# Kernel tuning notes

Hardware: AMD Instinct MI355X
Metric: run time of the kernel (lower is better)

## Reference

```python
import jax, jax.numpy as jnp
import numpy as np

D = 768      # hidden_size
H = 12       # num_head
HD = D // H  # head_dim
LN_EPS = 1e-5


def setup_inputs() -> dict:
    key = jax.random.key(0)
    ks = jax.random.split(key, 9)
    N, S = 4, 2048
    s = 0.02
    return {
        "hidden_state": jax.random.normal(ks[0], (N, S, D), dtype=jnp.float32),
        "key_padding_mask": jax.random.randint(ks[1], (N, S), 0, 2, dtype=jnp.int64),
        "Wq": jax.random.normal(ks[2], (D, D), dtype=jnp.float32) * s,
        "Wk": jax.random.normal(ks[3], (D, D), dtype=jnp.float32) * s,
        "Wv": jax.random.normal(ks[4], (D, D), dtype=jnp.float32) * s,
        "Wo": jax.random.normal(ks[5], (D, D), dtype=jnp.float32) * s,
        "W1": jax.random.normal(ks[6], (4 * D, D), dtype=jnp.float32) * s,
        "W2": jax.random.normal(ks[7], (D, 4 * D), dtype=jnp.float32) * s,
        "ln_g": jnp.ones((D,), dtype=jnp.float32),
        "ln_b": jnp.zeros((D,), dtype=jnp.float32),
    }


def _layernorm(x, g, b):
    mu = jnp.mean(x, axis=-1, keepdims=True)
    var = jnp.mean(jnp.square(x - mu), axis=-1, keepdims=True)
    return (x - mu) * jax.lax.rsqrt(var + LN_EPS) * g + b


def reference(hidden_state, key_padding_mask, Wq, Wk, Wv, Wo, W1, W2, ln_g, ln_b):
    x = hidden_state
    N, S, _ = x.shape
    # Note: original module projects K and V from `query` (self-attention).
    def proj(W):
        return (x @ W.T).reshape(N, S, H, HD).transpose(0, 2, 1, 3)  # [N,H,S,HD]
    Q, K, V = proj(Wq), proj(Wk), proj(Wv)
    scores = jnp.einsum("bhqd,bhkd->bhqk", Q, K)  # [N,H,S,S]
    # int mask: 0 marks padding positions -> masked with -inf
    pad = (key_padding_mask == 0)[:, None, None, :]  # [N,1,1,S]
    scores = jnp.where(pad, -jnp.inf, scores)
    attn = jax.nn.softmax(scores / np.sqrt(HD), axis=-1)
    ctx = jnp.einsum("bhqk,bhkd->bhqd", attn, V)
    ctx = ctx.transpose(0, 2, 1, 3).reshape(N, S, D)
    mha = ctx @ Wo.T
    # residual + LayerNorm (same LN params used twice, as in the original)
    n1 = _layernorm(x + mha, ln_g, ln_b)
    # FFN with exact GELU (torch nn.GELU default)
    f = jax.nn.gelu(n1 @ W1.T, approximate=False) @ W2.T
    return _layernorm(n1 + f, ln_g, ln_b)
```

## Files before the change

kernel.cpp:

```cpp
#include <hip/hip_runtime.h>
#include <math.h>

typedef unsigned short u16;
typedef unsigned int u32;
typedef __bf16 bf16x8 __attribute__((ext_vector_type(8)));
typedef float f32x4 __attribute__((ext_vector_type(4)));
typedef u32 u32x4 __attribute__((ext_vector_type(4)));

#define NB 4
#define SS 2048
#define DD 768
#define HH 12
#define HD 64
#define ROWS (NB*SS)

__device__ __forceinline__ u16 f2bf(float f) {
    union { float f; unsigned u; } v; v.f = f;
    unsigned r = v.u + 0x7fffu + ((v.u >> 16) & 1u);
    return (u16)(r >> 16);
}
__device__ __forceinline__ u32 fas(float f) { union { float f; u32 u; } v; v.f = f; return v.u; }

__device__ __forceinline__ void gl_lds16(const void* g, void* l) {
    __builtin_amdgcn_global_load_lds((__attribute__((address_space(1))) void*)(g),
                                     (__attribute__((address_space(3))) void*)(l),
                                     16, 0, 0);
}

__global__ __launch_bounds__(256) void prep_kernel(
        const float* __restrict__ X, const float* __restrict__ Wq,
        const float* __restrict__ Wk, const float* __restrict__ Wv,
        const float* __restrict__ Wo, const float* __restrict__ W1,
        const float* __restrict__ W2,
        u16* __restrict__ Xb, u16* __restrict__ Wqkvb, u16* __restrict__ Wob,
        u16* __restrict__ W1b, u16* __restrict__ W2b) {
    const int blk = blockIdx.x, tid = threadIdx.x;
    const float* src; u16* dst; int idx;
    if (blk < 6144)       { src = X;  dst = Xb;               idx = blk * 1024 + tid * 4; }
    else if (blk < 6720)  { src = Wq; dst = Wqkvb;            idx = (blk - 6144) * 1024 + tid * 4; }
    else if (blk < 7296)  { src = Wk; dst = Wqkvb + DD * DD;  idx = (blk - 6720) * 1024 + tid * 4; }
    else if (blk < 7872)  { src = Wv; dst = Wqkvb + 2*DD*DD;  idx = (blk - 7296) * 1024 + tid * 4; }
    else if (blk < 8448)  { src = Wo; dst = Wob;              idx = (blk - 7872) * 1024 + tid * 4; }
    else if (blk < 10752) { src = W1; dst = W1b;              idx = (blk - 8448) * 1024 + tid * 4; }
    else                  { src = W2; dst = W2b;              idx = (blk - 10752) * 1024 + tid * 4; }
    float4 v = *(const float4*)&src[idx];
    ushort4 o;
    o.x = f2bf(v.x); o.y = f2bf(v.y); o.z = f2bf(v.z); o.w = f2bf(v.w);
    *(ushort4*)&dst[idx] = o;
}

__global__ __launch_bounds__(256) void scan_kernel(const int* __restrict__ mask,
                                                   int* __restrict__ cidx,
                                                   int* __restrict__ cnt) {
    const int b = blockIdx.x, tid = threadIdx.x;
    const int lane = tid & 63, wave = tid >> 6;
    const int base = b * SS + tid * 8;
    int4 m0 = *(const int4*)&mask[base];
    int4 m1 = *(const int4*)&mask[base + 4];
    int v[8] = { m0.x != 0, m0.y != 0, m0.z != 0, m0.w != 0,
                 m1.x != 0, m1.y != 0, m1.z != 0, m1.w != 0 };
    int own = 0;
#pragma unroll
    for (int i = 0; i < 8; ++i) own += v[i];
    int inc = own;
#pragma unroll
    for (int o = 1; o < 64; o <<= 1) {
        int n = __shfl_up(inc, o);
        if (lane >= o) inc += n;
    }
    __shared__ int wsum[4];
    if (lane == 63) wsum[wave] = inc;
    __syncthreads();
    int wbase = 0;
#pragma unroll
    for (int w = 0; w < 4; ++w) wbase += (w < wave) ? wsum[w] : 0;
    int pos = wbase + inc - own;
    int o8[8];
#pragma unroll
    for (int i = 0; i < 8; ++i) { o8[i] = v[i] ? pos : -1; pos += v[i]; }
    *(int4*)&cidx[base]     = make_int4(o8[0], o8[1], o8[2], o8[3]);
    *(int4*)&cidx[base + 4] = make_int4(o8[4], o8[5], o8[6], o8[7]);
    if (tid == 255) cnt[b] = wbase + inc;
}

template <int EPI, int BN>
__global__ __launch_bounds__(256) void gemm_bt(const u16* __restrict__ A,
                                               const u16* __restrict__ B,
                                               int M, int N, int K,
                                               void* __restrict__ out,
                                               const void* __restrict__ aux,
                                               u16* __restrict__ Qb,
                                               u16* __restrict__ Kb,
                                               u16* __restrict__ Vb,
                                               const int* __restrict__ cidx) {
    __shared__ __align__(16) u16 lA[128 * 64];
    __shared__ __align__(16) u16 lB[BN * 64];
    constexpr int MI = (BN == 128) ? 4 : 2;
    const int tid = threadIdx.x;
    const int lane = tid & 63, wave = tid >> 6;
    const int quad = lane >> 4, lc = lane & 15;
    const int xcd = blockIdx.x & 7, loc = blockIdx.x >> 3;
    const int mb = xcd * 8 + (loc & 7), nb = loc >> 3;
    const int m0 = mb * 128, n0 = nb * BN;
    const int wrow = (BN == 128) ? (wave >> 1) * 64 : wave * 32;
    const int wcol = (BN == 128) ? (wave & 1) * 64 : 0;
    const int swz = lc & 7;

    f32x4 acc[MI][4] = {};

    for (int kb = 0; kb < K; kb += 64) {
        __syncthreads();
#pragma unroll
        for (int p0 = 0; p0 < 1024; p0 += 256) {
            int p = p0 + tid, row = p >> 3, cl = (p & 7) ^ (row & 7);
            gl_lds16(A + (size_t)(m0 + row) * K + kb + cl * 8, &lA[(size_t)(p0 + wave * 64) * 8]);
        }
#pragma unroll
        for (int p0 = 0; p0 < BN * 8; p0 += 256) {
            int p = p0 + tid, row = p >> 3, cl = (p & 7) ^ (row & 7);
            gl_lds16(B + (size_t)(n0 + row) * K + kb + cl * 8, &lB[(size_t)(p0 + wave * 64) * 8]);
        }
        __syncthreads();
#pragma unroll
        for (int k2 = 0; k2 < 2; ++k2) {
            bf16x8 af[MI], bfr[4];
#pragma unroll
            for (int t = 0; t < MI; ++t)
                af[t] = *(const bf16x8*)&lA[(wrow + t * 16 + lc) * 64 + ((quad + k2 * 4) ^ swz) * 8];
#pragma unroll
            for (int t = 0; t < 4; ++t)
                bfr[t] = *(const bf16x8*)&lB[(wcol + t * 16 + lc) * 64 + ((quad + k2 * 4) ^ swz) * 8];
#pragma unroll
            for (int mi = 0; mi < MI; ++mi)
#pragma unroll
                for (int ni = 0; ni < 4; ++ni)
                    acc[mi][ni] = __builtin_amdgcn_mfma_f32_16x16x32_bf16(af[mi], bfr[ni],
                                                                         acc[mi][ni], 0, 0, 0);
        }
    }

#pragma unroll
    for (int mi = 0; mi < MI; ++mi) {
        int csa[4];
        if constexpr (EPI == 0) {
            int mbase = m0 + wrow + mi * 16 + quad * 4;
            int4 cs4 = *(const int4*)&cidx[(mbase >> 11) * SS + (mbase & 2047)];
            csa[0] = cs4.x; csa[1] = cs4.y; csa[2] = cs4.z; csa[3] = cs4.w;
        }
#pragma unroll
        for (int r = 0; r < 4; ++r) {
            int m = m0 + wrow + mi * 16 + quad * 4 + r;
#pragma unroll
            for (int ni = 0; ni < 4; ++ni) {
                int n = n0 + wcol + ni * 16 + lc;
                float v = acc[mi][ni][r];
                if constexpr (EPI == 0) {
                    int b = m >> 11, s = m & 2047;
                    int which = n / DD, rem = n - which * DD;
                    int h = rem >> 6, d = rem & 63;
                    u16* dst = which == 0 ? Qb : (which == 1 ? Kb : Vb);
                    int sidx = which == 0 ? s : csa[r];
                    if (sidx >= 0)
                        dst[((((size_t)b * HH + h) * SS + sidx) << 6) + d] = f2bf(v);
                } else if constexpr (EPI == 1) {
                    float u = v * fmaf(v * v, 0.035677408f, 0.7978845608f);
                    float e = __builtin_amdgcn_exp2f(u * 2.885390082f);
                    float g = v - v * __builtin_amdgcn_rcpf(e + 1.0f);
                    ((u16*)out)[(size_t)m * N + n] = f2bf(g);
                } else if constexpr (EPI == 2) {
                    ((float*)out)[(size_t)m * N + n] =
                        v + ((const float*)aux)[(size_t)m * N + n];
                } else {
                    ((float*)out)[(size_t)m * N + n] =
                        v + (float)(((const __bf16*)aux)[(size_t)m * N + n]);
                }
            }
        }
    }
}

__global__ __launch_bounds__(256) void transpose_v(const u16* __restrict__ V,
                                                   u16* __restrict__ Vt,
                                                   const int* __restrict__ cnt) {
    __shared__ u16 t[32][33];
    int bh = blockIdx.z;
    int c = cnt[bh / HH];
    int cr = (c + 63) & ~63;
    int s0 = blockIdx.x * 32, d0 = blockIdx.y * 32;
    if (s0 >= cr) return;
    const u16* vb = V + (size_t)bh * SS * HD;
    u16* vtb = Vt + (size_t)bh * HD * SS;
    int tx = threadIdx.x & 31, ty = threadIdx.x >> 5;
#pragma unroll
    for (int i = 0; i < 32; i += 8) {
        int s = s0 + ty + i;
        t[ty + i][tx] = (s < c) ? vb[(size_t)s * HD + d0 + tx] : (u16)0;
    }
    __syncthreads();
#pragma unroll
    for (int i = 0; i < 32; i += 8) vtb[(size_t)(d0 + ty + i) * SS + s0 + tx] = t[tx][ty + i];
}

__global__ __launch_bounds__(256, 3) void attn_kernel(const u16* __restrict__ Q,
                                                      const u16* __restrict__ K,
                                                      const u16* __restrict__ Vt,
                                                      const int* __restrict__ cntg,
                                                      u16* __restrict__ Ctx) {
    __shared__ __align__(16) u16 lK[2][4096];
    __shared__ __align__(16) u16 lV[2][4096];
    const int tid = threadIdx.x, lane = tid & 63, wave = tid >> 6;
    const int quad = lane >> 4, lc = lane & 15;
    const int bh = blockIdx.x % (NB * HH);
    const int b = bh / HH, h = bh - b * HH;
    const int q0 = (blockIdx.x / (NB * HH)) * 128;
    const u16* Qg = Q + ((size_t)bh * SS + q0 + wave * 32) * HD;
    const u16* Kg = K + (size_t)bh * SS * HD;
    const u16* Vg = Vt + (size_t)bh * HD * SS;
    const int sw = lc & 7;
    const int cnt = cntg[b];
    const int nt = (cnt + 63) >> 6;

    const int srow = tid >> 3, scl = (tid & 7) ^ (srow & 7);
    const int srow2 = (256 + tid) >> 3, scl2 = (tid & 7) ^ (srow2 & 7);

    auto stage = [&](int bi, int j0) {
        gl_lds16(Kg + (size_t)(j0 + srow) * HD + scl * 8,   &lK[bi][(size_t)(wave * 64) * 8]);
        gl_lds16(Kg + (size_t)(j0 + srow2) * HD + scl2 * 8, &lK[bi][(size_t)(256 + wave * 64) * 8]);
        gl_lds16(Vg + (size_t)srow * SS + j0 + scl * 8,     &lV[bi][(size_t)(wave * 64) * 8]);
        gl_lds16(Vg + (size_t)srow2 * SS + j0 + scl2 * 8,   &lV[bi][(size_t)(256 + wave * 64) * 8]);
    };

    bf16x8 qf[2][2];
#pragma unroll
    for (int mi = 0; mi < 2; ++mi)
#pragma unroll
        for (int k2 = 0; k2 < 2; ++k2)
            qf[mi][k2] = *(const bf16x8*)(Qg + (size_t)(mi * 16 + lc) * HD + k2 * 32 + quad * 8);

    bf16x8 onesf;
#pragma unroll
    for (int i = 0; i < 8; ++i) onesf[i] = (__bf16)1.0f;

    f32x4 oacc[2][4] = {};
    f32x4 lsum[2] = {};

    stage(0, 0);
    for (int t = 0; t < nt; ++t) {
        const int cur = t & 1;
        if (t < nt - 1) {
            stage(cur ^ 1, (t + 1) * 64);
            __builtin_amdgcn_sched_barrier(0);
            asm volatile("s_waitcnt vmcnt(4)" ::: "memory");
        } else {
            __builtin_amdgcn_sched_barrier(0);
            asm volatile("s_waitcnt vmcnt(0)" ::: "memory");
        }
        __builtin_amdgcn_sched_barrier(0);
        __builtin_amdgcn_s_barrier();
        __builtin_amdgcn_sched_barrier(0);

        const u16* bK = &lK[cur][0];
        const u16* bV = &lV[cur][0];

        f32x4 sacc[2][4] = {};
        __builtin_amdgcn_s_setprio(1);
#pragma unroll
        for (int k2 = 0; k2 < 2; ++k2) {
            bf16x8 kf[4];
#pragma unroll
            for (int ni = 0; ni < 4; ++ni)
                kf[ni] = *(const bf16x8*)&bK[(ni * 16 + lc) * 64 + ((quad + k2 * 4) ^ sw) * 8];
#pragma unroll
            for (int ni = 0; ni < 4; ++ni) {
                sacc[0][ni] = __builtin_amdgcn_mfma_f32_16x16x32_bf16(kf[ni], qf[0][k2], sacc[0][ni], 0, 0, 0);
                sacc[1][ni] = __builtin_amdgcn_mfma_f32_16x16x32_bf16(kf[ni], qf[1][k2], sacc[1][ni], 0, 0, 0);
            }
        }
        __builtin_amdgcn_s_setprio(0);

        const int kb_ = cnt - t * 64;
        const bool part = kb_ < 64;
        u32 pa[2][4], pb[2][4];
#pragma unroll
        for (int ni = 0; ni < 4; ++ni) {
#pragma unroll
            for (int mi = 0; mi < 2; ++mi) {
#pragma unroll
                for (int r = 0; r < 4; ++r) {
                    float e = __builtin_amdgcn_exp2f(sacc[mi][ni][r] * 0.180336880f);
                    if (part) e = (ni * 16 + quad * 4 + r < kb_) ? e : 0.0f;
                    sacc[mi][ni][r] = e;
                }
                pa[mi][ni] = __builtin_amdgcn_perm(fas(sacc[mi][ni][1]), fas(sacc[mi][ni][0]), 0x07060302);
                pb[mi][ni] = __builtin_amdgcn_perm(fas(sacc[mi][ni][3]), fas(sacc[mi][ni][2]), 0x07060302);
            }
        }

        bf16x8 pf[2][2];
#pragma unroll
        for (int mi = 0; mi < 2; ++mi)
#pragma unroll
            for (int k2 = 0; k2 < 2; ++k2) {
                u32 xa = pa[mi][2 * k2], ya = pa[mi][2 * k2 + 1];
                u32 xb = pb[mi][2 * k2], yb = pb[mi][2 * k2 + 1];
                asm("v_permlane32_swap_b32 %0, %1" : "+v"(xa), "+v"(ya));
                asm("v_permlane16_swap_b32 %0, %1" : "+v"(xa), "+v"(ya));
                asm("v_permlane32_swap_b32 %0, %1" : "+v"(xb), "+v"(yb));
                asm("v_permlane16_swap_b32 %0, %1" : "+v"(xb), "+v"(yb));
                u32x4 pw = { xa, xb, ya, yb };
                pf[mi][k2] = __builtin_bit_cast(bf16x8, pw);
            }

        __builtin_amdgcn_s_setprio(1);
#pragma unroll
        for (int k2 = 0; k2 < 2; ++k2) {
            lsum[0] = __builtin_amdgcn_mfma_f32_16x16x32_bf16(pf[0][k2], onesf, lsum[0], 0, 0, 0);
            lsum[1] = __builtin_amdgcn_mfma_f32_16x16x32_bf16(pf[1][k2], onesf, lsum[1], 0, 0, 0);
#pragma unroll
            for (int ni = 0; ni < 4; ++ni) {
                bf16x8 vf = *(const bf16x8*)&bV[(ni * 16 + lc) * 64 + ((quad + k2 * 4) ^ sw) * 8];
                oacc[0][ni] = __builtin_amdgcn_mfma_f32_16x16x32_bf16(pf[0][k2], vf, oacc[0][ni], 0, 0, 0);
                oacc[1][ni] = __builtin_amdgcn_mfma_f32_16x16x32_bf16(pf[1][k2], vf, oacc[1][ni], 0, 0, 0);
            }
        }
        __builtin_amdgcn_s_setprio(0);

        __builtin_amdgcn_sched_barrier(0);
        __builtin_amdgcn_s_barrier();
    }

#pragma unroll
    for (int mi = 0; mi < 2; ++mi)
#pragma unroll
        for (int r = 0; r < 4; ++r) {
            float inv = 1.0f / lsum[mi][r];
            int s = q0 + wave * 32 + mi * 16 + quad * 4 + r;
            size_t base = ((size_t)(b * SS + s)) * DD + h * HD;
#pragma unroll
            for (int ni = 0; ni < 4; ++ni)
                Ctx[base + ni * 16 + lc] = f2bf(oacc[mi][ni][r] * inv);
        }
}

__global__ __launch_bounds__(256) void ln_kernel(const float* __restrict__ in,
                                                 const float* __restrict__ g,
                                                 const float* __restrict__ bb,
                                                 u16* __restrict__ out_bf,
                                                 float* __restrict__ out_f) {
    const int row = blockIdx.x, tid = threadIdx.x;
    const float* x = in + (size_t)row * DD;
    float v0 = x[tid], v1 = x[tid + 256], v2 = x[tid + 512];
    float s = v0 + v1 + v2;
    float q = v0 * v0 + v1 * v1 + v2 * v2;
#pragma unroll
    for (int o = 1; o < 64; o <<= 1) {
        s += __shfl_xor(s, o);
        q += __shfl_xor(q, o);
    }
    __shared__ float rs[4], rq[4];
    int wave = tid >> 6;
    if ((tid & 63) == 0) { rs[wave] = s; rq[wave] = q; }
    __syncthreads();
    s = rs[0] + rs[1] + rs[2] + rs[3];
    q = rq[0] + rq[1] + rq[2] + rq[3];
    float mu = s * (1.0f / DD);
    float var = q * (1.0f / DD) - mu * mu;
    float rstd = rsqrtf(var + 1e-5f);
#pragma unroll
    for (int j = 0; j < 3; ++j) {
        int col = tid + j * 256;
        float v = (j == 0 ? v0 : (j == 1 ? v1 : v2));
        float y = (v - mu) * rstd * g[col] + bb[col];
        if (out_bf) out_bf[(size_t)row * DD + col] = f2bf(y);
        if (out_f) out_f[(size_t)row * DD + col] = y;
    }
}

extern "C" void kernel_launch(void* const* d_in, const int* in_sizes, int n_in,
                              void* d_out, int out_size, void* d_ws, size_t ws_size,
                              hipStream_t stream) {
    const float* X    = (const float*)d_in[0];
    const int*   mask = (const int*)d_in[1];
    const float* Wq   = (const float*)d_in[2];
    const float* Wk   = (const float*)d_in[3];
    const float* Wv   = (const float*)d_in[4];
    const float* Wo   = (const float*)d_in[5];
    const float* W1   = (const float*)d_in[6];
    const float* W2   = (const float*)d_in[7];
    const float* ln_g = (const float*)d_in[8];
    const float* ln_b = (const float*)d_in[9];
    float* out = (float*)d_out;

    char* ws = (char*)d_ws;
    size_t off = 0;
    auto alloc = [&](size_t bytes) {
        void* p = ws + off;
        off += (bytes + 255) & ~(size_t)255;
        return p;
    };
    u16*   Xbf   = (u16*)alloc((size_t)ROWS * DD * 2);
    u16*   Wqkvb = (u16*)alloc((size_t)3 * DD * DD * 2);
    u16*   Wob   = (u16*)alloc((size_t)DD * DD * 2);
    u16*   W1b   = (u16*)alloc((size_t)4 * DD * DD * 2);
    u16*   W2b   = (u16*)alloc((size_t)4 * DD * DD * 2);
    int*   cidx  = (int*)alloc((size_t)NB * SS * 4);
    int*   cnt   = (int*)alloc(256);
    u16*   Qb    = (u16*)alloc((size_t)ROWS * DD * 2);
    u16*   Kb    = (u16*)alloc((size_t)ROWS * DD * 2);
    u16*   Vb    = (u16*)alloc((size_t)ROWS * DD * 2);
    u16*   Vtb   = (u16*)alloc((size_t)ROWS * DD * 2);
    float* resid = (float*)alloc((size_t)ROWS * DD * 4);
    u16*   n1b   = (u16*)alloc((size_t)ROWS * DD * 2);
    u16*   Gb    = Qb;
    u16*   Ctxb  = Xbf;
    float* h2    = resid;

    prep_kernel<<<dim3(13056), dim3(256), 0, stream>>>(
        X, Wq, Wk, Wv, Wo, W1, W2,
        Xbf, Wqkvb, Wob, W1b, W2b);

    scan_kernel<<<dim3(NB), dim3(256), 0, stream>>>(mask, cidx, cnt);

    gemm_bt<0, 128><<<dim3((3 * DD / 128) * (ROWS / 128)), dim3(256), 0, stream>>>(
        Xbf, Wqkvb, ROWS, 3 * DD, DD, nullptr, nullptr, Qb, Kb, Vb, cidx);

    transpose_v<<<dim3(SS / 32, HD / 32, NB * HH), dim3(256), 0, stream>>>(Vb, Vtb, cnt);

    attn_kernel<<<dim3((SS / 128) * (NB * HH)), dim3(256), 0, stream>>>(
        Qb, Kb, Vtb, cnt, Ctxb);

    gemm_bt<2, 64><<<dim3((DD / 64) * (ROWS / 128)), dim3(256), 0, stream>>>(
        Ctxb, Wob, ROWS, DD, DD, resid, X, nullptr, nullptr, nullptr, nullptr);

    ln_kernel<<<dim3(ROWS), dim3(256), 0, stream>>>(resid, ln_g, ln_b, n1b, nullptr);

    gemm_bt<1, 128><<<dim3((4 * DD / 128) * (ROWS / 128)), dim3(256), 0, stream>>>(
        n1b, W1b, ROWS, 4 * DD, DD, Gb, nullptr, nullptr, nullptr, nullptr, nullptr);

    gemm_bt<3, 64><<<dim3((DD / 64) * (ROWS / 128)), dim3(256), 0, stream>>>(
        Gb, W2b, ROWS, DD, 4 * DD, h2, n1b, nullptr, nullptr, nullptr, nullptr);

    ln_kernel<<<dim3(ROWS), dim3(256), 0, stream>>>(h2, ln_g, ln_b, nullptr, out);
}
```

Baseline: 337.3 us.

## Double-buffer GEMM LDS tiles with async prefetch and fold mask scan into prep

The GEMM main loop now uses two LDS buffers. The next K-tile is issued via global_load_lds before computing the current one, with explicit vmcnt waits, barriers, and raised wave priority around the MFMA block. This is meant to hide global-to-LDS latency that the single-buffer loop exposed. The mask prefix-scan also moves into extra blocks of the prep kernel, removing one launch. The cost is double the LDS per block, which may lower occupancy, and hand-counted vmcnt values that must match the number of loads issued per stage.

```diff
diff --git a/kernel.cpp b/kernel.cpp
--- a/kernel.cpp
+++ b/kernel.cpp
@@ -31,9 +31,10 @@
         const float* __restrict__ X, const float* __restrict__ Wq,
         const float* __restrict__ Wk, const float* __restrict__ Wv,
         const float* __restrict__ Wo, const float* __restrict__ W1,
-        const float* __restrict__ W2,
+        const float* __restrict__ W2, const int* __restrict__ mask,
         u16* __restrict__ Xb, u16* __restrict__ Wqkvb, u16* __restrict__ Wob,
-        u16* __restrict__ W1b, u16* __restrict__ W2b) {
+        u16* __restrict__ W1b, u16* __restrict__ W2b,
+        int* __restrict__ cidx, int* __restrict__ cnt) {
     const int blk = blockIdx.x, tid = threadIdx.x;
     const float* src; u16* dst; int idx;
     if (blk < 6144)       { src = X;  dst = Xb;               idx = blk * 1024 + tid * 4; }
@@ -42,45 +43,43 @@
     else if (blk < 7872)  { src = Wv; dst = Wqkvb + 2*DD*DD;  idx = (blk - 7296) * 1024 + tid * 4; }
     else if (blk < 8448)  { src = Wo; dst = Wob;              idx = (blk - 7872) * 1024 + tid * 4; }
     else if (blk < 10752) { src = W1; dst = W1b;              idx = (blk - 8448) * 1024 + tid * 4; }
-    else                  { src = W2; dst = W2b;              idx = (blk - 10752) * 1024 + tid * 4; }
+    else if (blk < 13056) { src = W2; dst = W2b;              idx = (blk - 10752) * 1024 + tid * 4; }
+    else {
+        const int b = blk - 13056;
+        const int lane = tid & 63, wave = tid >> 6;
+        const int base = b * SS + tid * 8;
+        int4 m0 = *(const int4*)&mask[base];
+        int4 m1 = *(const int4*)&mask[base + 4];
+        int v[8] = { m0.x != 0, m0.y != 0, m0.z != 0, m0.w != 0,
+                     m1.x != 0, m1.y != 0, m1.z != 0, m1.w != 0 };
+        int own = 0;
+#pragma unroll
+        for (int i = 0; i < 8; ++i) own += v[i];
+        int inc = own;
+#pragma unroll
+        for (int o = 1; o < 64; o <<= 1) {
+            int n = __shfl_up(inc, o);
+            if (lane >= o) inc += n;
+        }
+        __shared__ int wsum[4];
+        if (lane == 63) wsum[wave] = inc;
+        __syncthreads();
+        int wbase = 0;
+#pragma unroll
+        for (int w = 0; w < 4; ++w) wbase += (w < wave) ? wsum[w] : 0;
+        int pos = wbase + inc - own;
+        int o8[8];
+#pragma unroll
+        for (int i = 0; i < 8; ++i) { o8[i] = v[i] ? pos : -1; pos += v[i]; }
+        *(int4*)&cidx[base]     = make_int4(o8[0], o8[1], o8[2], o8[3]);
+        *(int4*)&cidx[base + 4] = make_int4(o8[4], o8[5], o8[6], o8[7]);
+        if (tid == 255) cnt[b] = wbase + inc;
+        return;
+    }
     float4 v = *(const float4*)&src[idx];
     ushort4 o;
     o.x = f2bf(v.x); o.y = f2bf(v.y); o.z = f2bf(v.z); o.w = f2bf(v.w);
     *(ushort4*)&dst[idx] = o;
-}
-
-__global__ __launch_bounds__(256) void scan_kernel(const int* __restrict__ mask,
-                                                   int* __restrict__ cidx,
-                                                   int* __restrict__ cnt) {
-    const int b = blockIdx.x, tid = threadIdx.x;
-    const int lane = tid & 63, wave = tid >> 6;
-    const int base = b * SS + tid * 8;
-    int4 m0 = *(const int4*)&mask[base];
-    int4 m1 = *(const int4*)&mask[base + 4];
-    int v[8] = { m0.x != 0, m0.y != 0, m0.z != 0, m0.w != 0,
-                 m1.x != 0, m1.y != 0, m1.z != 0, m1.w != 0 };
-    int own = 0;
-#pragma unroll
-    for (int i = 0; i < 8; ++i) own += v[i];
-    int inc = own;
-#pragma unroll
-    for (int o = 1; o < 64; o <<= 1) {
-        int n = __shfl_up(inc, o);
-        if (lane >= o) inc += n;
-    }
-    __shared__ int wsum[4];
-    if (lane == 63) wsum[wave] = inc;
-    __syncthreads();
-    int wbase = 0;
-#pragma unroll
-    for (int w = 0; w < 4; ++w) wbase += (w < wave) ? wsum[w] : 0;
-    int pos = wbase + inc - own;
-    int o8[8];
-#pragma unroll
-    for (int i = 0; i < 8; ++i) { o8[i] = v[i] ? pos : -1; pos += v[i]; }
-    *(int4*)&cidx[base]     = make_int4(o8[0], o8[1], o8[2], o8[3]);
-    *(int4*)&cidx[base + 4] = make_int4(o8[4], o8[5], o8[6], o8[7]);
-    if (tid == 255) cnt[b] = wbase + inc;
 }
 
 template <int EPI, int BN>
@@ -93,8 +92,8 @@
                                                u16* __restrict__ Kb,
                                                u16* __restrict__ Vb,
                                                const int* __restrict__ cidx) {
-    __shared__ __align__(16) u16 lA[128 * 64];
-    __shared__ __align__(16) u16 lB[BN * 64];
+    __shared__ __align__(16) u16 lA[2][128 * 64];
+    __shared__ __align__(16) u16 lB[2][BN * 64];
     constexpr int MI = (BN == 128) ? 4 : 2;
     const int tid = threadIdx.x;
     const int lane = tid & 63, wave = tid >> 6;
@@ -106,37 +105,60 @@
     const int wcol = (BN == 128) ? (wave & 1) * 64 : 0;
     const int swz = lc & 7;
 
-    f32x4 acc[MI][4] = {};
-
-    for (int kb = 0; kb < K; kb += 64) {
-        __syncthreads();
+    auto stage = [&](int bi, int kb) {
 #pragma unroll
         for (int p0 = 0; p0 < 1024; p0 += 256) {
             int p = p0 + tid, row = p >> 3, cl = (p & 7) ^ (row & 7);
-            gl_lds16(A + (size_t)(m0 + row) * K + kb + cl * 8, &lA[(size_t)(p0 + wave * 64) * 8]);
+            gl_lds16(A + (size_t)(m0 + row) * K + kb + cl * 8, &lA[bi][(size_t)(p0 + wave * 64) * 8]);
         }
 #pragma unroll
         for (int p0 = 0; p0 < BN * 8; p0 += 256) {
             int p = p0 + tid, row = p >> 3, cl = (p & 7) ^ (row & 7);
-            gl_lds16(B + (size_t)(n0 + row) * K + kb + cl * 8, &lB[(size_t)(p0 + wave * 64) * 8]);
-        }
-        __syncthreads();
+            gl_lds16(B + (size_t)(n0 + row) * K + kb + cl * 8, &lB[bi][(size_t)(p0 + wave * 64) * 8]);
+        }
+    };
+
+    f32x4 acc[MI][4] = {};
+    const int KT = K >> 6;
+
+    stage(0, 0);
+    for (int t = 0; t < KT; ++t) {
+        const int cur = t & 1;
+        if (t < KT - 1) {
+            stage(cur ^ 1, (t + 1) << 6);
+            __builtin_amdgcn_sched_barrier(0);
+            if constexpr (BN == 128) asm volatile("s_waitcnt vmcnt(8)" ::: "memory");
+            else                     asm volatile("s_waitcnt vmcnt(6)" ::: "memory");
+        } else {
+            __builtin_amdgcn_sched_barrier(0);
+            asm volatile("s_waitcnt vmcnt(0)" ::: "memory");
+        }
+        __builtin_amdgcn_sched_barrier(0);
+        __builtin_amdgcn_s_barrier();
+        __builtin_amdgcn_sched_barrier(0);
+
+        const u16* bA = &lA[cur][0];
+        const u16* bB = &lB[cur][0];
 #pragma unroll
         for (int k2 = 0; k2 < 2; ++k2) {
             bf16x8 af[MI], bfr[4];
 #pragma unroll
-            for (int t = 0; t < MI; ++t)
-                af[t] = *(const bf16x8*)&lA[(wrow + t * 16 + lc) * 64 + ((quad + k2 * 4) ^ swz) * 8];
-#pragma unroll
-            for (int t = 0; t < 4; ++t)
-                bfr[t] = *(const bf16x8*)&lB[(wcol + t * 16 + lc) * 64 + ((quad + k2 * 4) ^ swz) * 8];
+            for (int t_ = 0; t_ < MI; ++t_)
+                af[t_] = *(const bf16x8*)&bA[(wrow + t_ * 16 + lc) * 64 + ((quad + k2 * 4) ^ swz) * 8];
+#pragma unroll
+            for (int t_ = 0; t_ < 4; ++t_)
+                bfr[t_] = *(const bf16x8*)&bB[(wcol + t_ * 16 + lc) * 64 + ((quad + k2 * 4) ^ swz) * 8];
+            __builtin_amdgcn_s_setprio(1);
 #pragma unroll
             for (int mi = 0; mi < MI; ++mi)
 #pragma unroll
                 for (int ni = 0; ni < 4; ++ni)
                     acc[mi][ni] = __builtin_amdgcn_mfma_f32_16x16x32_bf16(af[mi], bfr[ni],
                                                                          acc[mi][ni], 0, 0, 0);
-        }
+            __builtin_amdgcn_s_setprio(0);
+        }
+        __builtin_amdgcn_sched_barrier(0);
+        __builtin_amdgcn_s_barrier();
     }
 
 #pragma unroll
@@ -415,11 +437,9 @@
     u16*   Ctxb  = Xbf;
     float* h2    = resid;
 
-    prep_kernel<<<dim3(13056), dim3(256), 0, stream>>>(
-        X, Wq, Wk, Wv, Wo, W1, W2,
-        Xbf, Wqkvb, Wob, W1b, W2b);
-
-    scan_kernel<<<dim3(NB), dim3(256), 0, stream>>>(mask, cidx, cnt);
+    prep_kernel<<<dim3(13056 + NB), dim3(256), 0, stream>>>(
+        X, Wq, Wk, Wv, Wo, W1, W2, mask,
+        Xbf, Wqkvb, Wob, W1b, W2b, cidx, cnt);
 
     gemm_bt<0, 128><<<dim3((3 * DD / 128) * (ROWS / 128)), dim3(256), 0, stream>>>(
         Xbf, Wqkvb, ROWS, 3 * DD, DD, nullptr, nullptr, Qb, Kb, Vb, cidx);
```

After: 345.5 us. +2.4%, slower.
